# Performance work log

Hardware: AMD Instinct MI355X
Metric: run time of the kernel (lower is better)

## Reference

```python
import jax, jax.numpy as jnp
import numpy as np

N = 100000
E = 1600000
IN_DIM = 64
HID = 64
OUT = 64
BN_EPS = 1e-5


def setup_inputs() -> dict:
    key = jax.random.key(0)
    ks = jax.random.split(key, 16)
    x = jax.random.normal(ks[0], (N, IN_DIM), dtype=jnp.float32)
    edge_index = jax.random.randint(ks[1], (2, E), 0, N, dtype=jnp.int64)
    def lin(k, fan_in, fan_out):
        bound = 1.0 / np.sqrt(fan_in)
        kw, kb = jax.random.split(k)
        W = jax.random.uniform(kw, (fan_in, fan_out), jnp.float32, -bound, bound)
        b = jax.random.uniform(kb, (fan_out,), jnp.float32, -bound, bound)
        return W, b
    W1, b1 = lin(ks[2], IN_DIM, HID)
    W2, b2 = lin(ks[3], HID, HID)
    g1 = jnp.ones((HID,), jnp.float32)
    bt1 = jnp.zeros((HID,), jnp.float32)
    eps1 = jnp.zeros((), jnp.float32)
    W3, b3 = lin(ks[4], HID, HID)
    W4, b4 = lin(ks[5], HID, OUT)
    g2 = jnp.ones((OUT,), jnp.float32)
    bt2 = jnp.zeros((OUT,), jnp.float32)
    eps2 = jnp.zeros((), jnp.float32)
    return {"x": x, "edge_index": edge_index,
            "W1": W1, "b1": b1, "W2": W2, "b2": b2, "g1": g1, "bt1": bt1, "eps1": eps1,
            "W3": W3, "b3": b3, "W4": W4, "b4": b4, "g2": g2, "bt2": bt2, "eps2": eps2}


def _bn(h, gamma, beta):
    # BatchNorm1d in training mode: per-feature batch stats, biased variance
    mean = jnp.mean(h, axis=0)
    var = jnp.mean((h - mean) ** 2, axis=0)
    return (h - mean) * jax.lax.rsqrt(var + BN_EPS) * gamma + beta


def _gin_conv(x, src, dst, eps, Wa, ba, Wb, bb, gamma, beta):
    # scatter-add aggregation: sum_{j in N(i)} x_j
    agg = jax.ops.segment_sum(x[src], dst, num_segments=N)  # [N, D]
    h = (1.0 + eps) * x + agg
    h = jax.nn.relu(h @ Wa + ba)
    h = jax.nn.relu(h @ Wb + bb)
    return _bn(h, gamma, beta)


def reference(x, edge_index, W1, b1, W2, b2, g1, bt1, eps1, W3, b3, W4, b4, g2, bt2, eps2):
    src, dst = edge_index[0], edge_index[1]
    h = _gin_conv(x, src, dst, eps1, W1, b1, W2, b2, g1, bt1)
    h = _gin_conv(h, src, dst, eps2, W3, b3, W4, b4, g2, bt2)
    return (h, jax.nn.log_softmax(h, axis=-1))
```

## Files before the change

### kernel.cpp

```cpp
#include <hip/hip_runtime.h>

#define NN 100000
#define NE 1600000

typedef __attribute__((ext_vector_type(8))) short short8;
typedef __attribute__((ext_vector_type(4))) float floatx4;

__device__ __forceinline__ unsigned short f2bf(float f) {
  unsigned u = __float_as_uint(f);
  u += 0x7fffu + ((u >> 16) & 1u);
  return (unsigned short)(u >> 16);
}
__device__ __forceinline__ float bf2f(unsigned short b) {
  return __uint_as_float(((unsigned)b) << 16);
}

__global__ __launch_bounds__(256) void k_cvtW(const float* __restrict__ W1,
                                              const float* __restrict__ W2,
                                              const float* __restrict__ W3,
                                              const float* __restrict__ W4,
                                              unsigned short* __restrict__ Wb) {
  int i = blockIdx.x * 256 + threadIdx.x;
  Wb[i] = f2bf(W1[i]);
  Wb[4096 + i] = f2bf(W2[i]);
  Wb[8192 + i] = f2bf(W3[i]);
  Wb[12288 + i] = f2bf(W4[i]);
}

__global__ __launch_bounds__(256) void k_fill(const int* __restrict__ src,
                                              const int* __restrict__ dst,
                                              int* __restrict__ cursor,
                                              int* __restrict__ ell) {
  int e = blockIdx.x * 256 + threadIdx.x;
  int d = dst[e];
  int p = atomicAdd(&cursor[d * 16], 1);
  if (p < 64) ell[d * 64 + p] = src[e];
}

template <int MODE>
__global__ __launch_bounds__(256) void k_gather(const float* __restrict__ xf,
                                                const unsigned short* __restrict__ xb,
                                                const int* __restrict__ deg16,
                                                const int* __restrict__ ell,
                                                const float* __restrict__ eps,
                                                const float* __restrict__ AB,
                                                unsigned short* __restrict__ agg) {
  const int lane = threadIdx.x & 31;
  const int slot = threadIdx.x >> 5;
  const int n = blockIdx.x * 8 + slot;
  const int fo = 2 * lane;
  float A0 = 1.0f, B0 = 0.0f, A1 = 1.0f, B1 = 0.0f;
  if (MODE) { A0 = AB[fo]; B0 = AB[64 + fo]; A1 = AB[fo + 1]; B1 = AB[64 + fo + 1]; }
  float s0, s1;
  if (MODE) {
    ushort2 u = *(const ushort2*)(xb + n * 64 + fo);
    s0 = fmaf(bf2f(u.x), A0, B0);
    s1 = fmaf(bf2f(u.y), A1, B1);
  } else {
    float2 u = *(const float2*)(xf + n * 64 + fo);
    s0 = u.x;
    s1 = u.y;
  }
  const float es = 1.0f + eps[0];
  float a0 = es * s0, a1 = es * s1;
  float b0 = 0, b1 = 0, c0 = 0, c1 = 0, d0 = 0, d1 = 0;
  const int cnt = deg16[n * 16];
  const int* row = ell + n * 64;
  const int4* r4 = (const int4*)row;
  int j = 0;
  for (; j + 4 <= cnt; j += 4) {
    int4 s4 = r4[j >> 2];
    if (MODE) {
      ushort2 u0 = *(const ushort2*)(xb + s4.x * 64 + fo);
      ushort2 u1 = *(const ushort2*)(xb + s4.y * 64 + fo);
      ushort2 u2 = *(const ushort2*)(xb + s4.z * 64 + fo);
      ushort2 u3 = *(const ushort2*)(xb + s4.w * 64 + fo);
      a0 = fmaf(bf2f(u0.x), A0, a0); a1 = fmaf(bf2f(u0.y), A1, a1);
      b0 = fmaf(bf2f(u1.x), A0, b0); b1 = fmaf(bf2f(u1.y), A1, b1);
      c0 = fmaf(bf2f(u2.x), A0, c0); c1 = fmaf(bf2f(u2.y), A1, c1);
      d0 = fmaf(bf2f(u3.x), A0, d0); d1 = fmaf(bf2f(u3.y), A1, d1);
      a0 += B0; a1 += B1; b0 += B0; b1 += B1;
      c0 += B0; c1 += B1; d0 += B0; d1 += B1;
    } else {
      float2 u0 = *(const float2*)(xf + s4.x * 64 + fo);
      float2 u1 = *(const float2*)(xf + s4.y * 64 + fo);
      float2 u2 = *(const float2*)(xf + s4.z * 64 + fo);
      float2 u3 = *(const float2*)(xf + s4.w * 64 + fo);
      a0 += u0.x; a1 += u0.y;
      b0 += u1.x; b1 += u1.y;
      c0 += u2.x; c1 += u2.y;
      d0 += u3.x; d1 += u3.y;
    }
  }
  for (; j < cnt; j++) {
    int s = row[j];
    if (MODE) {
      ushort2 u = *(const ushort2*)(xb + s * 64 + fo);
      a0 += fmaf(bf2f(u.x), A0, B0);
      a1 += fmaf(bf2f(u.y), A1, B1);
    } else {
      float2 u = *(const float2*)(xf + s * 64 + fo);
      a0 += u.x;
      a1 += u.y;
    }
  }
  float r0 = (a0 + b0) + (c0 + d0);
  float r1 = (a1 + b1) + (c1 + d1);
  ushort2 st;
  st.x = f2bf(r0);
  st.y = f2bf(r1);
  *(ushort2*)(agg + n * 64 + fo) = st;
}

__global__ __launch_bounds__(256) void k_mlp_mfma(
    const unsigned short* __restrict__ agg, const unsigned short* __restrict__ Wab,
    const float* __restrict__ ba, const float* __restrict__ bb,
    unsigned short* __restrict__ h2, double* __restrict__ stats) {
  const int l = threadIdx.x & 63;
  const int wv = threadIdx.x >> 6;
  const int l16 = l & 15, quad = l >> 4;

  short8 wfa[4][2], wfb[4][2];
#pragma unroll
  for (int c = 0; c < 4; c++)
#pragma unroll
    for (int t = 0; t < 2; t++)
#pragma unroll
      for (int j = 0; j < 8; j++) {
        int k = t * 32 + quad * 8 + j, nn = c * 16 + l16;
        wfa[c][t][j] = (short)Wab[k * 64 + nn];
        wfb[c][t][j] = (short)Wab[4096 + k * 64 + nn];
      }
  float bia[4], bib[4];
#pragma unroll
  for (int c = 0; c < 4; c++) { bia[c] = ba[c * 16 + l16]; bib[c] = bb[c * 16 + l16]; }

  __shared__ float Hs[4][16][68];
  __shared__ float sS[4][64], sQ[4][64];
  float ssum[4] = {0, 0, 0, 0}, ssq[4] = {0, 0, 0, 0};

  const int totw = gridDim.x * 4;
  for (int tile = blockIdx.x * 4 + wv; tile < NN / 16; tile += totw) {
    const int r0 = tile * 16;
    const unsigned short* ap = agg + (r0 + l16) * 64 + quad * 8;
    short8 a0 = *(const short8*)ap;
    short8 a1 = *(const short8*)(ap + 32);
#pragma unroll
    for (int c = 0; c < 4; c++) {
      floatx4 acc = {0.f, 0.f, 0.f, 0.f};
      acc = __builtin_amdgcn_mfma_f32_16x16x32_bf16(a0, wfa[c][0], acc, 0, 0, 0);
      acc = __builtin_amdgcn_mfma_f32_16x16x32_bf16(a1, wfa[c][1], acc, 0, 0, 0);
#pragma unroll
      for (int r = 0; r < 4; r++)
        Hs[wv][quad * 4 + r][c * 16 + l16] = fmaxf(acc[r] + bia[c], 0.0f);
    }
    short8 a20, a21;
#pragma unroll
    for (int j = 0; j < 8; j++) {
      a20[j] = (short)f2bf(Hs[wv][l16][quad * 8 + j]);
      a21[j] = (short)f2bf(Hs[wv][l16][32 + quad * 8 + j]);
    }
#pragma unroll
    for (int c = 0; c < 4; c++) {
      floatx4 acc = {0.f, 0.f, 0.f, 0.f};
      acc = __builtin_amdgcn_mfma_f32_16x16x32_bf16(a20, wfb[c][0], acc, 0, 0, 0);
      acc = __builtin_amdgcn_mfma_f32_16x16x32_bf16(a21, wfb[c][1], acc, 0, 0, 0);
#pragma unroll
      for (int r = 0; r < 4; r++) {
        float v = fmaxf(acc[r] + bib[c], 0.0f);
        h2[(r0 + quad * 4 + r) * 64 + c * 16 + l16] = f2bf(v);
        ssum[c] += v;
        ssq[c] += v * v;
      }
    }
  }
#pragma unroll
  for (int c = 0; c < 4; c++) {
    float s = ssum[c], q = ssq[c];
    s += __shfl_xor(s, 16, 64); s += __shfl_xor(s, 32, 64);
    q += __shfl_xor(q, 16, 64); q += __shfl_xor(q, 32, 64);
    if (quad == 0) { sS[wv][c * 16 + l16] = s; sQ[wv][c * 16 + l16] = q; }
  }
  __syncthreads();
  if (threadIdx.x < 64) {
    int ff = threadIdx.x;
    float s = sS[0][ff] + sS[1][ff] + sS[2][ff] + sS[3][ff];
    float q = sQ[0][ff] + sQ[1][ff] + sQ[2][ff] + sQ[3][ff];
    unsafeAtomicAdd(&stats[ff], (double)s);
    unsafeAtomicAdd(&stats[64 + ff], (double)q);
  }
}

__global__ void k_bnfin(const double* __restrict__ stats, const float* __restrict__ gam,
                        const float* __restrict__ bet, float* __restrict__ AB) {
  int f = threadIdx.x;
  double mean = stats[f] * (1.0 / NN);
  double var = stats[64 + f] * (1.0 / NN) - mean * mean;
  if (var < 0.0) var = 0.0;
  float rstd = (float)(1.0 / sqrt(var + 1e-5));
  float A = gam[f] * rstd;
  float B = bet[f] - (float)mean * A;
  AB[f] = A;
  AB[64 + f] = B;
}

__global__ __launch_bounds__(256) void k_out(const unsigned short* __restrict__ h2,
                                             const float* __restrict__ AB,
                                             float* __restrict__ out) {
  int f = threadIdx.x & 63;
  int n = blockIdx.x * 4 + (threadIdx.x >> 6);
  float v = bf2f(h2[n * 64 + f]);
  float h = fmaf(v, AB[f], AB[64 + f]);
  float m = h;
#pragma unroll
  for (int off = 32; off; off >>= 1) m = fmaxf(m, __shfl_xor(m, off, 64));
  float e = expf(h - m);
  float ssum = e;
#pragma unroll
  for (int off = 32; off; off >>= 1) ssum += __shfl_xor(ssum, off, 64);
  float lsm = (h - m) - logf(ssum);
  out[n * 64 + f] = h;
  out[(size_t)NN * 64 + n * 64 + f] = lsm;
}

extern "C" void kernel_launch(void* const* d_in, const int* in_sizes, int n_in,
                              void* d_out, int out_size, void* d_ws, size_t ws_size,
                              hipStream_t stream) {
  const float* x = (const float*)d_in[0];
  const int* ei = (const int*)d_in[1];
  const float* W1 = (const float*)d_in[2];
  const float* b1 = (const float*)d_in[3];
  const float* W2 = (const float*)d_in[4];
  const float* b2 = (const float*)d_in[5];
  const float* g1 = (const float*)d_in[6];
  const float* bt1 = (const float*)d_in[7];
  const float* e1 = (const float*)d_in[8];
  const float* W3 = (const float*)d_in[9];
  const float* b3 = (const float*)d_in[10];
  const float* W4 = (const float*)d_in[11];
  const float* b4 = (const float*)d_in[12];
  const float* g2 = (const float*)d_in[13];
  const float* bt2 = (const float*)d_in[14];
  const float* e2 = (const float*)d_in[15];
  const int* src = ei;
  const int* dst = ei + NE;

  char* ws = (char*)d_ws;
  unsigned short* aggb = (unsigned short*)(ws);
  unsigned short* h2b = (unsigned short*)(ws + 12800000);
  int* ell = (int*)(ws + 25600000);
  int* cursor = (int*)(ws + 51200000);
  double* st1 = (double*)(ws + 57600000);
  double* st2 = (double*)(ws + 57601024);
  float* AB1 = (float*)(ws + 57602048);
  float* AB2 = (float*)(ws + 57602560);
  unsigned short* Wbb = (unsigned short*)(ws + 57603072);
  float* out = (float*)d_out;

  hipMemsetAsync(ws + 57600000, 0, 2048, stream);
  hipMemsetAsync(cursor, 0, 6400000, stream);

  k_cvtW<<<16, 256, 0, stream>>>(W1, W2, W3, W4, Wbb);

  k_fill<<<NE / 256, 256, 0, stream>>>(src, dst, cursor, ell);

  k_gather<0><<<NN / 8, 256, 0, stream>>>(x, nullptr, cursor, ell, e1, nullptr, aggb);
  k_mlp_mfma<<<391, 256, 0, stream>>>(aggb, Wbb, b1, b2, h2b, st1);
  k_bnfin<<<1, 64, 0, stream>>>(st1, g1, bt1, AB1);
  k_gather<1><<<NN / 8, 256, 0, stream>>>(nullptr, h2b, cursor, ell, e2, AB1, aggb);
  k_mlp_mfma<<<391, 256, 0, stream>>>(aggb, Wbb + 8192, b3, b4, h2b, st2);
  k_bnfin<<<1, 64, 0, stream>>>(st2, g2, bt2, AB2);
  k_out<<<NN / 4, 256, 0, stream>>>(h2b, AB2, out);
}
```

Measured before the change: 389.2 us.

## Build ELL adjacency via bucketed counting sort instead of global atomics

Replaces the single atomic fill kernel, which did one global atomicAdd per edge on padded per-node cursors and needed a 6.4MB memset, with a multi-pass bucket sort. Edges are first histogrammed into 256 destination-node buckets, the counts are prefix-scanned and the edges scattered into an intermediate array. Each bucket is then filled into the ELL layout using shared-memory atomics. This removes global atomic contention and the big memset, at the cost of four extra launches and an extra pass over the edges through memory. The gather kernels now read a compact degree array.

```diff
diff --git a/kernel.cpp b/kernel.cpp
--- a/kernel.cpp
+++ b/kernel.cpp
@@ -2,6 +2,9 @@
 
 #define NN 100000
 #define NE 1600000
+#define NB 256
+#define BSZ 391
+#define EB 782
 
 typedef __attribute__((ext_vector_type(8))) short short8;
 typedef __attribute__((ext_vector_type(4))) float floatx4;
@@ -27,20 +30,104 @@
   Wb[12288 + i] = f2bf(W4[i]);
 }
 
-__global__ __launch_bounds__(256) void k_fill(const int* __restrict__ src,
-                                              const int* __restrict__ dst,
-                                              int* __restrict__ cursor,
-                                              int* __restrict__ ell) {
-  int e = blockIdx.x * 256 + threadIdx.x;
-  int d = dst[e];
-  int p = atomicAdd(&cursor[d * 16], 1);
-  if (p < 64) ell[d * 64 + p] = src[e];
+__global__ __launch_bounds__(256) void k_phist(const int* __restrict__ dst,
+                                               int* __restrict__ blockHist) {
+  __shared__ int h[NB];
+  h[threadIdx.x] = 0;
+  __syncthreads();
+  int base = blockIdx.x * 2048;
+#pragma unroll
+  for (int i = 0; i < 8; i++) {
+    int e = base + i * 256 + threadIdx.x;
+    if (e < NE) atomicAdd(&h[dst[e] / BSZ], 1);
+  }
+  __syncthreads();
+  blockHist[blockIdx.x * NB + threadIdx.x] = h[threadIdx.x];
+}
+
+__global__ __launch_bounds__(1024) void k_colscan(const int* __restrict__ blockHist,
+                                                  int* __restrict__ offsL,
+                                                  int* __restrict__ colTot) {
+  __shared__ int sh[1024];
+  int c = blockIdx.x, t = threadIdx.x;
+  int v = (t < EB) ? blockHist[t * NB + c] : 0;
+  sh[t] = v;
+  __syncthreads();
+  for (int off = 1; off < 1024; off <<= 1) {
+    int u = (t >= off) ? sh[t - off] : 0;
+    __syncthreads();
+    sh[t] += u;
+    __syncthreads();
+  }
+  if (t < EB) offsL[t * NB + c] = sh[t] - v;
+  if (t == EB - 1) colTot[c] = sh[t];
+}
+
+__global__ __launch_bounds__(256) void k_basescan(const int* __restrict__ colTot,
+                                                  int* __restrict__ base) {
+  __shared__ int sh[256];
+  int t = threadIdx.x;
+  int v = colTot[t];
+  sh[t] = v;
+  __syncthreads();
+  for (int off = 1; off < 256; off <<= 1) {
+    int u = (t >= off) ? sh[t - off] : 0;
+    __syncthreads();
+    sh[t] += u;
+    __syncthreads();
+  }
+  base[t] = sh[t] - v;
+  if (t == 255) base[256] = sh[255];
+}
+
+__global__ __launch_bounds__(256) void k_escat(const int* __restrict__ src,
+                                               const int* __restrict__ dst,
+                                               const int* __restrict__ offsL,
+                                               const int* __restrict__ base,
+                                               int2* __restrict__ ed) {
+  __shared__ int h[NB];
+  h[threadIdx.x] = 0;
+  __syncthreads();
+  int eb = blockIdx.x * 2048;
+  const int* ofs = offsL + blockIdx.x * NB;
+#pragma unroll
+  for (int i = 0; i < 8; i++) {
+    int e = eb + i * 256 + threadIdx.x;
+    if (e < NE) {
+      int d = dst[e];
+      int c = d / BSZ;
+      int r = atomicAdd(&h[c], 1);
+      ed[base[c] + ofs[c] + r] = make_int2(src[e], d);
+    }
+  }
+}
+
+__global__ __launch_bounds__(256) void k_ellfill(const int2* __restrict__ ed,
+                                                 const int* __restrict__ base,
+                                                 int* __restrict__ ell,
+                                                 int* __restrict__ deg) {
+  __shared__ int cur[BSZ];
+  int c = blockIdx.x;
+  for (int i = threadIdx.x; i < BSZ; i += 256) cur[i] = 0;
+  __syncthreads();
+  int lo = base[c], hi = base[c + 1];
+  int n0 = c * BSZ;
+  for (int e = lo + threadIdx.x; e < hi; e += 256) {
+    int2 sd = ed[e];
+    int slot = atomicAdd(&cur[sd.y - n0], 1);
+    if (slot < 64) ell[sd.y * 64 + slot] = sd.x;
+  }
+  __syncthreads();
+  for (int i = threadIdx.x; i < BSZ; i += 256) {
+    int n = n0 + i;
+    if (n < NN) deg[n] = min(cur[i], 64);
+  }
 }
 
 template <int MODE>
 __global__ __launch_bounds__(256) void k_gather(const float* __restrict__ xf,
                                                 const unsigned short* __restrict__ xb,
-                                                const int* __restrict__ deg16,
+                                                const int* __restrict__ deg,
                                                 const int* __restrict__ ell,
                                                 const float* __restrict__ eps,
                                                 const float* __restrict__ AB,
@@ -64,7 +151,7 @@
   const float es = 1.0f + eps[0];
   float a0 = es * s0, a1 = es * s1;
   float b0 = 0, b1 = 0, c0 = 0, c1 = 0, d0 = 0, d1 = 0;
-  const int cnt = deg16[n * 16];
+  const int cnt = deg[n];
   const int* row = ell + n * 64;
   const int4* r4 = (const int4*)row;
   int j = 0;
@@ -249,25 +336,33 @@
   unsigned short* aggb = (unsigned short*)(ws);
   unsigned short* h2b = (unsigned short*)(ws + 12800000);
   int* ell = (int*)(ws + 25600000);
-  int* cursor = (int*)(ws + 51200000);
-  double* st1 = (double*)(ws + 57600000);
-  double* st2 = (double*)(ws + 57601024);
-  float* AB1 = (float*)(ws + 57602048);
-  float* AB2 = (float*)(ws + 57602560);
-  unsigned short* Wbb = (unsigned short*)(ws + 57603072);
+  int2* ed = (int2*)(ws + 51200000);
+  int* blockHist = (int*)(ws + 64000000);
+  int* offsL = (int*)(ws + 64800768);
+  int* colTot = (int*)(ws + 65601536);
+  int* base = (int*)(ws + 65602560);
+  int* deg = (int*)(ws + 65603600);
+  double* st1 = (double*)(ws + 66003600);
+  double* st2 = (double*)(ws + 66004624);
+  float* AB1 = (float*)(ws + 66005648);
+  float* AB2 = (float*)(ws + 66006160);
+  unsigned short* Wbb = (unsigned short*)(ws + 66006672);
   float* out = (float*)d_out;
 
-  hipMemsetAsync(ws + 57600000, 0, 2048, stream);
-  hipMemsetAsync(cursor, 0, 6400000, stream);
+  hipMemsetAsync(ws + 66003600, 0, 2048, stream);
 
   k_cvtW<<<16, 256, 0, stream>>>(W1, W2, W3, W4, Wbb);
 
-  k_fill<<<NE / 256, 256, 0, stream>>>(src, dst, cursor, ell);
-
-  k_gather<0><<<NN / 8, 256, 0, stream>>>(x, nullptr, cursor, ell, e1, nullptr, aggb);
+  k_phist<<<EB, 256, 0, stream>>>(dst, blockHist);
+  k_colscan<<<NB, 1024, 0, stream>>>(blockHist, offsL, colTot);
+  k_basescan<<<1, 256, 0, stream>>>(colTot, base);
+  k_escat<<<EB, 256, 0, stream>>>(src, dst, offsL, base, ed);
+  k_ellfill<<<NB, 256, 0, stream>>>(ed, base, ell, deg);
+
+  k_gather<0><<<NN / 8, 256, 0, stream>>>(x, nullptr, deg, ell, e1, nullptr, aggb);
   k_mlp_mfma<<<391, 256, 0, stream>>>(aggb, Wbb, b1, b2, h2b, st1);
   k_bnfin<<<1, 64, 0, stream>>>(st1, g1, bt1, AB1);
-  k_gather<1><<<NN / 8, 256, 0, stream>>>(nullptr, h2b, cursor, ell, e2, AB1, aggb);
+  k_gather<1><<<NN / 8, 256, 0, stream>>>(nullptr, h2b, deg, ell, e2, AB1, aggb);
   k_mlp_mfma<<<391, 256, 0, stream>>>(aggb, Wbb + 8192, b3, b4, h2b, st2);
   k_bnfin<<<1, 64, 0, stream>>>(st2, g2, bt2, AB2);
   k_out<<<NN / 4, 256, 0, stream>>>(h2b, AB2, out);
```

Result: faster. 317.2 us (-18.5%).
